# Kernel tuning notes

Measured on AMD Instinct MI355X. Metric: run time of the kernel, lower is better.

## Reference

```python
import jax, jax.numpy as jnp
import numpy as np

N = 50000      # nodes
E = 800000     # edges (before self-loops)
IN = 256       # in_dim
HID = 64       # hidden_dim per head
HEADS = 4
OUT = 256      # out_dim
NEG_SLOPE = 0.2


def setup_inputs() -> dict:
    key = jax.random.key(0)
    ks = jax.random.split(key, 12)
    s = 0.1
    return {
        "x": jax.random.normal(ks[0], (N, IN), jnp.float32),
        "edge_index": jax.random.randint(ks[1], (2, E), 0, N, dtype=jnp.int32),
        # layer 1: GATConv(IN, HID, heads=HEADS, concat=True)
        "W1": jax.random.normal(ks[2], (IN, HEADS * HID), jnp.float32) * s,
        "att_src1": jax.random.normal(ks[3], (HEADS, HID), jnp.float32) * s,
        "att_dst1": jax.random.normal(ks[4], (HEADS, HID), jnp.float32) * s,
        "b1": jnp.zeros((HEADS * HID,), jnp.float32),
        # layer 2: GATConv(HEADS*HID, OUT, heads=1, concat=False)
        "W2": jax.random.normal(ks[5], (HEADS * HID, OUT), jnp.float32) * s,
        "att_src2": jax.random.normal(ks[6], (1, OUT), jnp.float32) * s,
        "att_dst2": jax.random.normal(ks[7], (1, OUT), jnp.float32) * s,
        "b2": jnp.zeros((OUT,), jnp.float32),
    }


def _gat_layer(x, src, dst, W, a_src, a_dst, b, heads, concat):
    n = x.shape[0]
    h = (x @ W).reshape(n, heads, -1)                     # [N,H,F]
    al_s = jnp.einsum('nhf,hf->nh', h, a_src)             # [N,H]
    al_d = jnp.einsum('nhf,hf->nh', h, a_dst)
    e = jax.nn.leaky_relu(al_s[src] + al_d[dst], NEG_SLOPE)  # [E,H]
    # segment softmax over incoming edges of each dst node
    m = jax.lax.stop_gradient(jax.ops.segment_max(e, dst, num_segments=n))
    ex = jnp.exp(e - m[dst])
    denom = jax.ops.segment_sum(ex, dst, num_segments=n)
    alpha = ex / (denom[dst] + 1e-16)                     # [E,H]
    out = jax.ops.segment_sum(h[src] * alpha[:, :, None], dst, num_segments=n)  # [N,H,F]
    out = out.reshape(n, -1) if concat else out.mean(axis=1)
    return out + b


def reference(x, edge_index, W1, att_src1, att_dst1, b1, W2, att_src2, att_dst2, b2):
    n = x.shape[0]
    loop = jnp.arange(n, dtype=edge_index.dtype)
    ei = jnp.concatenate([edge_index, jnp.stack([loop, loop])], axis=1)  # add self loops
    src, dst = ei[0], ei[1]
    h = _gat_layer(x, src, dst, W1, att_src1, att_dst1, b1, HEADS, True)
    h = jax.nn.elu(h)
    out = _gat_layer(h, src, dst, W2, att_src2, att_dst2, b2, 1, False)
    return out
```

## Files before the change

kernel.cpp:

```cpp
#include <hip/hip_runtime.h>
#include <math.h>

#define IN_DIM 256
#define FDIM 256
#define HEADS 4
#define NEG 0.2f
#define MAXD 96

typedef __attribute__((ext_vector_type(8))) short bf16x8;
typedef __attribute__((ext_vector_type(8))) unsigned short u16x8;
typedef __attribute__((ext_vector_type(4))) float f32x4;

__device__ __forceinline__ float leaky(float x){ return x > 0.f ? x : NEG * x; }

__device__ __forceinline__ unsigned short f2bf(float f){
  unsigned int u = __float_as_uint(f);
  unsigned int r = u + 0x7fffu + ((u >> 16) & 1u);
  return (unsigned short)(r >> 16);
}
__device__ __forceinline__ float bf2f(unsigned short s){
  return __uint_as_float(((unsigned int)s) << 16);
}

__device__ __forceinline__ float4 bcast4(float4 v){
  return make_float4(__shfl(v.x,0,64), __shfl(v.y,0,64), __shfl(v.z,0,64), __shfl(v.w,0,64));
}
__device__ __forceinline__ float comp4(float4 v, int h){
  return h==0 ? v.x : h==1 ? v.y : h==2 ? v.z : v.w;
}

__device__ __forceinline__ void gld_lds16(const void* g, void* l){
  __builtin_amdgcn_global_load_lds((const __attribute__((address_space(1))) unsigned int*)g,
                                   (__attribute__((address_space(3))) unsigned int*)l, 16, 0, 0);
}

__global__ void k_wthist(const float* __restrict__ W1, unsigned short* __restrict__ W1t,
                         const float* __restrict__ W2, unsigned short* __restrict__ W2t,
                         const int* __restrict__ dst, int* __restrict__ deg, int E){
  int b = blockIdx.x;
  if (b < 32){
    __shared__ float tile[64][65];
    const float* W = (b < 16) ? W1 : W2;
    unsigned short* Wt = (b < 16) ? W1t : W2t;
    int bb = b & 15;
    int tk = (bb >> 2) * 64, tn = (bb & 3) * 64;
    int t = threadIdx.x;
    int cr = t >> 6, cc = t & 63;
    #pragma unroll
    for (int r = 0; r < 16; ++r){
      int k = r * 4 + cr;
      tile[k][cc] = W[(size_t)(tk + k) * 256 + tn + cc];
    }
    __syncthreads();
    #pragma unroll
    for (int r = 0; r < 16; ++r){
      int nn = r * 4 + cr;
      Wt[(size_t)(tn + nn) * 256 + tk + cc] = f2bf(tile[cc][nn]);
    }
  } else {
    int e = (b - 32) * 256 + threadIdx.x;
    if (e < E) atomicAdd(&deg[dst[e]], 1);
  }
}

__global__ void k_scanA(const int* __restrict__ deg, int* tmp, int* partials, int n){
  __shared__ int sm[256];
  int i = blockIdx.x * 256 + threadIdx.x;
  int v = (i < n) ? deg[i] + 1 : 0;
  sm[threadIdx.x] = v; __syncthreads();
  for (int off = 1; off < 256; off <<= 1){
    int x = (threadIdx.x >= off) ? sm[threadIdx.x - off] : 0;
    __syncthreads();
    sm[threadIdx.x] += x;
    __syncthreads();
  }
  if (i < n) tmp[i] = sm[threadIdx.x];
  if (threadIdx.x == 255) partials[blockIdx.x] = sm[255];
}

__global__ void k_scanC(const int* __restrict__ tmp, const int* __restrict__ deg,
                        const int* __restrict__ partials, int* rowptr, int n, int nb){
  __shared__ int ws[4];
  int bid = blockIdx.x, t = threadIdx.x;
  int lane = t & 63, w = t >> 6;
  int v = (t < bid && t < nb) ? partials[t] : 0;
  #pragma unroll
  for (int off = 32; off >= 1; off >>= 1) v += __shfl_down(v, off, 64);
  if (lane == 0) ws[w] = v;
  __syncthreads();
  int prefix = ws[0] + ws[1] + ws[2] + ws[3];
  int i = bid * 256 + t;
  if (i < n){
    int incl = tmp[i] + prefix;
    rowptr[i] = incl - (deg[i] + 1);
    if (i == n - 1) rowptr[n] = incl;
  }
}

__global__ void k_fill(const int* __restrict__ src, const int* __restrict__ dst,
                       const int* __restrict__ rowptr, int* fill, int* col, int E, int n){
  int e = blockIdx.x * blockDim.x + threadIdx.x;
  if (e < E + n){
    int s, d;
    if (e < E){ s = src[e]; d = dst[e]; } else { s = d = e - E; }
    int pos = atomicAdd(&fill[d], 1);
    col[rowptr[d] + pos] = s;
  }
}

__global__ __launch_bounds__(256) void k_gemm1(const float* __restrict__ X,
                                               const unsigned short* __restrict__ Bt,
                                               unsigned short* __restrict__ C, int n){
  __shared__ __align__(16) unsigned short sh[8192];
  unsigned short* As = sh;
  unsigned short* Bs = sh + 4096;
  int tid = threadIdx.x;
  int lane = tid & 63, wave = tid >> 6;
  int rowBase = blockIdx.x * 128, colBase = blockIdx.y * 128;
  int wr = (wave & 1) * 64, wc = (wave >> 1) * 64;

  f32x4 acc[4][4] = {};
  int c0 = tid, c1 = tid + 256;
  int r0 = c0 >> 2, kc0 = (c0 & 3) * 8;
  int r1 = c1 >> 2, kc1 = (c1 & 3) * 8;
  int m0 = lane & 15, kq = (lane >> 4) * 8;
  int ra = rowBase + r0; if (ra >= n) ra = n - 1;
  int rb = rowBase + r1; if (rb >= n) rb = n - 1;

  for (int k0 = 0; k0 < 256; k0 += 32){
    float4 va0 = *(const float4*)(X + (size_t)ra * 256 + k0 + kc0);
    float4 va1 = *(const float4*)(X + (size_t)ra * 256 + k0 + kc0 + 4);
    float4 vb0 = *(const float4*)(X + (size_t)rb * 256 + k0 + kc1);
    float4 vb1 = *(const float4*)(X + (size_t)rb * 256 + k0 + kc1 + 4);
    u16x8 sa, sb;
    sa[0]=f2bf(va0.x); sa[1]=f2bf(va0.y); sa[2]=f2bf(va0.z); sa[3]=f2bf(va0.w);
    sa[4]=f2bf(va1.x); sa[5]=f2bf(va1.y); sa[6]=f2bf(va1.z); sa[7]=f2bf(va1.w);
    sb[0]=f2bf(vb0.x); sb[1]=f2bf(vb0.y); sb[2]=f2bf(vb0.z); sb[3]=f2bf(vb0.w);
    sb[4]=f2bf(vb1.x); sb[5]=f2bf(vb1.y); sb[6]=f2bf(vb1.z); sb[7]=f2bf(vb1.w);
    *(u16x8*)(As + c0 * 8) = sa;
    *(u16x8*)(As + c1 * 8) = sb;
    gld_lds16(Bt + (size_t)(colBase + r0) * 256 + k0 + kc0, (char*)Bs + c0 * 16);
    gld_lds16(Bt + (size_t)(colBase + r1) * 256 + k0 + kc1, (char*)Bs + c1 * 16);
    __syncthreads();
    bf16x8 af[4], bfr[4];
    #pragma unroll
    for (int it = 0; it < 4; ++it)
      af[it] = *(const bf16x8*)(As + (wr + it * 16 + m0) * 32 + kq);
    #pragma unroll
    for (int jt = 0; jt < 4; ++jt)
      bfr[jt] = *(const bf16x8*)(Bs + (wc + jt * 16 + m0) * 32 + kq);
    #pragma unroll
    for (int it = 0; it < 4; ++it)
      #pragma unroll
      for (int jt = 0; jt < 4; ++jt)
        acc[it][jt] = __builtin_amdgcn_mfma_f32_16x16x32_bf16(af[it], bfr[jt], acc[it][jt], 0, 0, 0);
    __syncthreads();
  }
  int cq = lane >> 4, cm = lane & 15;
  #pragma unroll
  for (int p = 0; p < 2; ++p){
    if ((wave >> 1) == p){
      #pragma unroll
      for (int it = 0; it < 4; ++it)
        #pragma unroll
        for (int jt = 0; jt < 4; ++jt)
          #pragma unroll
          for (int r = 0; r < 4; ++r)
            sh[(wr + it * 16 + cq * 4 + r) * 64 + jt * 16 + cm] = f2bf(acc[it][jt][r]);
    }
    __syncthreads();
    #pragma unroll
    for (int q = 0; q < 4; ++q){
      int id = tid + q * 256;
      int r = id >> 3, sg = id & 7;
      u16x8 v = *(const u16x8*)(sh + r * 64 + sg * 8);
      *(u16x8*)(C + (size_t)(rowBase + r) * 256 + colBase + p * 64 + sg * 8) = v;
    }
    __syncthreads();
  }
}

__global__ __launch_bounds__(256) void k_gemm(const unsigned short* __restrict__ A,
                                              const unsigned short* __restrict__ Bt,
                                              unsigned short* __restrict__ C){
  __shared__ __align__(16) unsigned short sh[8192];
  unsigned short* As = sh;
  unsigned short* Bs = sh + 4096;
  int tid = threadIdx.x;
  int lane = tid & 63, wave = tid >> 6;
  int rowBase = blockIdx.x * 128, colBase = blockIdx.y * 128;
  int wr = (wave & 1) * 64, wc = (wave >> 1) * 64;

  f32x4 acc[4][4] = {};
  int c0 = tid, c1 = tid + 256;
  int r0 = c0 >> 2, kc0 = (c0 & 3) * 8;
  int r1 = c1 >> 2, kc1 = (c1 & 3) * 8;
  int m0 = lane & 15, kq = (lane >> 4) * 8;

  for (int k0 = 0; k0 < 256; k0 += 32){
    gld_lds16(A  + (size_t)(rowBase + r0) * 256 + k0 + kc0, (char*)As + c0 * 16);
    gld_lds16(A  + (size_t)(rowBase + r1) * 256 + k0 + kc1, (char*)As + c1 * 16);
    gld_lds16(Bt + (size_t)(colBase + r0) * 256 + k0 + kc0, (char*)Bs + c0 * 16);
    gld_lds16(Bt + (size_t)(colBase + r1) * 256 + k0 + kc1, (char*)Bs + c1 * 16);
    __syncthreads();
    bf16x8 af[4], bfr[4];
    #pragma unroll
    for (int it = 0; it < 4; ++it)
      af[it] = *(const bf16x8*)(As + (wr + it * 16 + m0) * 32 + kq);
    #pragma unroll
    for (int jt = 0; jt < 4; ++jt)
      bfr[jt] = *(const bf16x8*)(Bs + (wc + jt * 16 + m0) * 32 + kq);
    #pragma unroll
    for (int it = 0; it < 4; ++it)
      #pragma unroll
      for (int jt = 0; jt < 4; ++jt)
        acc[it][jt] = __builtin_amdgcn_mfma_f32_16x16x32_bf16(af[it], bfr[jt], acc[it][jt], 0, 0, 0);
    __syncthreads();
  }
  int cq = lane >> 4, cm = lane & 15;
  #pragma unroll
  for (int p = 0; p < 2; ++p){
    if ((wave >> 1) == p){
      #pragma unroll
      for (int it = 0; it < 4; ++it)
        #pragma unroll
        for (int jt = 0; jt < 4; ++jt)
          #pragma unroll
          for (int r = 0; r < 4; ++r)
            sh[(wr + it * 16 + cq * 4 + r) * 64 + jt * 16 + cm] = f2bf(acc[it][jt][r]);
    }
    __syncthreads();
    #pragma unroll
    for (int q = 0; q < 4; ++q){
      int id = tid + q * 256;
      int r = id >> 3, sg = id & 7;
      u16x8 v = *(const u16x8*)(sh + r * 64 + sg * 8);
      *(u16x8*)(C + (size_t)(rowBase + r) * 256 + colBase + p * 64 + sg * 8) = v;
    }
    __syncthreads();
  }
}

__global__ __launch_bounds__(256) void k_al4(const unsigned short* __restrict__ Hb,
                      const float* __restrict__ as_, const float* __restrict__ ad_,
                      float* als, float* ald, int n){
  int wave = threadIdx.x >> 6, lane = threadIdx.x & 63;
  int i = blockIdx.x * 4 + wave; if (i >= n) i = n - 1;
  int f = lane * 4;
  ushort4 hv = *(const ushort4*)(Hb + (size_t)i * FDIM + f);
  float4 av = *(const float4*)(as_ + f);
  float4 dv = *(const float4*)(ad_ + f);
  float h0 = bf2f(hv.x), h1 = bf2f(hv.y), h2 = bf2f(hv.z), h3 = bf2f(hv.w);
  float ps = h0*av.x + h1*av.y + h2*av.z + h3*av.w;
  float pd = h0*dv.x + h1*dv.y + h2*dv.z + h3*dv.w;
  #pragma unroll
  for (int off = 8; off >= 1; off >>= 1){
    ps += __shfl_down(ps, off, 16);
    pd += __shfl_down(pd, off, 16);
  }
  if ((lane & 15) == 0){
    int h = lane >> 4;
    als[i * HEADS + h] = ps; ald[i * HEADS + h] = pd;
  }
}

__global__ __launch_bounds__(256) void k_al1(const unsigned short* __restrict__ Hb,
                      const float* __restrict__ as_, const float* __restrict__ ad_,
                      float* als, float* ald, int n){
  int wave = threadIdx.x >> 6, lane = threadIdx.x & 63;
  int i = blockIdx.x * 4 + wave; if (i >= n) i = n - 1;
  int f = lane * 4;
  ushort4 hv = *(const ushort4*)(Hb + (size_t)i * FDIM + f);
  float4 av = *(const float4*)(as_ + f);
  float4 dv = *(const float4*)(ad_ + f);
  float h0 = bf2f(hv.x), h1 = bf2f(hv.y), h2 = bf2f(hv.z), h3 = bf2f(hv.w);
  float ps = h0*av.x + h1*av.y + h2*av.z + h3*av.w;
  float pd = h0*dv.x + h1*dv.y + h2*dv.z + h3*dv.w;
  #pragma unroll
  for (int off = 32; off >= 1; off >>= 1){
    ps += __shfl_down(ps, off, 64);
    pd += __shfl_down(pd, off, 64);
  }
  if (lane == 0){ als[i] = ps; ald[i] = pd; }
}

__global__ __launch_bounds__(256) void k_agg1(const unsigned short* __restrict__ Hb,
    const float* __restrict__ als, const float* __restrict__ ald,
    const int* __restrict__ rowptr, const int* __restrict__ col,
    const float* __restrict__ b, unsigned short* __restrict__ outb, int i0, int nEnd){
  __shared__ __align__(16) int   colS[4][MAXD];
  __shared__ __align__(16) float wS[4][MAXD][4];
  int wave = threadIdx.x >> 6, t = threadIdx.x & 63;
  int i = i0 + blockIdx.x * 4 + wave; if (i >= nEnd) i = nEnd - 1;
  int start = rowptr[i];
  int deg = rowptr[i + 1] - start;
  float4 adv = *(const float4*)(ald + (size_t)i * 4);
  bool staged = (deg <= MAXD);

  float4 ls = make_float4(0.f, 0.f, 0.f, 0.f);
  if (staged){
    for (int j = t; j < deg; j += 64){
      int s = col[start + j];
      colS[wave][j] = s;
      float4 a = *(const float4*)(als + (size_t)s * 4);
      float4 w = make_float4(__expf(leaky(a.x + adv.x)), __expf(leaky(a.y + adv.y)),
                             __expf(leaky(a.z + adv.z)), __expf(leaky(a.w + adv.w)));
      *(float4*)(&wS[wave][j][0]) = w;
      ls.x += w.x; ls.y += w.y; ls.z += w.z; ls.w += w.w;
    }
  } else {
    for (int j = t; j < deg; j += 64){
      int s = col[start + j];
      float4 a = *(const float4*)(als + (size_t)s * 4);
      ls.x += __expf(leaky(a.x + adv.x)); ls.y += __expf(leaky(a.y + adv.y));
      ls.z += __expf(leaky(a.z + adv.z)); ls.w += __expf(leaky(a.w + adv.w));
    }
  }
  #pragma unroll
  for (int off = 32; off >= 1; off >>= 1) ls = make_float4(
      ls.x + __shfl_down(ls.x, off, 64), ls.y + __shfl_down(ls.y, off, 64),
      ls.z + __shfl_down(ls.z, off, 64), ls.w + __shfl_down(ls.w, off, 64));
  float4 d4 = bcast4(ls);
  __syncthreads();

  int e2 = t >> 5, l32 = t & 31;
  int h = l32 >> 3, f = l32 * 8;
  float inv = 1.f / (comp4(d4, h) + 1e-16f);
  const unsigned short* Hrow = Hb + f;
  float a0[8] = {0,0,0,0,0,0,0,0}, a1[8] = {0,0,0,0,0,0,0,0};
  if (staged){
    int j = 0;
    for (; j + 3 < deg; j += 4){
      int j0 = j + e2, j1 = j + 2 + e2;
      int s0 = colS[wave][j0], s1 = colS[wave][j1];
      float w0 = wS[wave][j0][h], w1 = wS[wave][j1][h];
      u16x8 h0 = *(const u16x8*)(Hrow + (size_t)s0 * FDIM);
      u16x8 h1 = *(const u16x8*)(Hrow + (size_t)s1 * FDIM);
      #pragma unroll
      for (int k = 0; k < 8; ++k){ a0[k] += bf2f(h0[k]) * w0; a1[k] += bf2f(h1[k]) * w1; }
    }
    for (; j < deg; j += 2){
      int jj = j + e2;
      if (jj < deg){
        int s = colS[wave][jj]; float w = wS[wave][jj][h];
        u16x8 hh = *(const u16x8*)(Hrow + (size_t)s * FDIM);
        #pragma unroll
        for (int k = 0; k < 8; ++k) a0[k] += bf2f(hh[k]) * w;
      }
    }
  } else {
    float adh = comp4(adv, h);
    for (int j = e2; j < deg; j += 2){
      int s = col[start + j];
      float w = __expf(leaky(als[(size_t)s * 4 + h] + adh));
      u16x8 hh = *(const u16x8*)(Hrow + (size_t)s * FDIM);
      #pragma unroll
      for (int k = 0; k < 8; ++k) a0[k] += bf2f(hh[k]) * w;
    }
  }
  float r[8];
  #pragma unroll
  for (int k = 0; k < 8; ++k){
    r[k] = a0[k] + a1[k];
    r[k] += __shfl_down(r[k], 32, 64);
  }
  if (t < 32){
    float4 bA = *(const float4*)(b + f);
    float4 bB = *(const float4*)(b + f + 4);
    float bb[8] = {bA.x, bA.y, bA.z, bA.w, bB.x, bB.y, bB.z, bB.w};
    u16x8 o;
    #pragma unroll
    for (int k = 0; k < 8; ++k){
      float v = r[k] * inv + bb[k];
      v = (v > 0.f) ? v : (__expf(v) - 1.f);
      o[k] = f2bf(v);
    }
    *(u16x8*)(outb + (size_t)i * FDIM + f) = o;
  }
}

__global__ __launch_bounds__(256) void k_agg2(const unsigned short* __restrict__ Hb,
    const float* __restrict__ als, const float* __restrict__ ald,
    const int* __restrict__ rowptr, const int* __restrict__ col,
    const float* __restrict__ b, float* __restrict__ out, int i0, int nEnd){
  __shared__ __align__(16) int   colS[4][MAXD];
  __shared__ __align__(16) float wS[4][MAXD];
  int wave = threadIdx.x >> 6, t = threadIdx.x & 63;
  int i = i0 + blockIdx.x * 4 + wave; if (i >= nEnd) i = nEnd - 1;
  int start = rowptr[i];
  int deg = rowptr[i + 1] - start;
  float adv = ald[i];
  bool staged = (deg <= MAXD);

  float ls = 0.f;
  if (staged){
    for (int j = t; j < deg; j += 64){
      int s = col[start + j];
      colS[wave][j] = s;
      float w = __expf(leaky(als[s] + adv));
      wS[wave][j] = w;
      ls += w;
    }
  } else {
    for (int j = t; j < deg; j += 64) ls += __expf(leaky(als[col[start + j]] + adv));
  }
  #pragma unroll
  for (int off = 32; off >= 1; off >>= 1) ls += __shfl_down(ls, off, 64);
  float inv = 1.f / (__shfl(ls, 0, 64) + 1e-16f);
  __syncthreads();

  int e2 = t >> 5, l32 = t & 31;
  int f = l32 * 8;
  const unsigned short* Hrow = Hb + f;
  float a0[8] = {0,0,0,0,0,0,0,0}, a1[8] = {0,0,0,0,0,0,0,0};
  if (staged){
    int j = 0;
    for (; j + 3 < deg; j += 4){
      int j0 = j + e2, j1 = j + 2 + e2;
      int s0 = colS[wave][j0], s1 = colS[wave][j1];
      float w0 = wS[wave][j0], w1 = wS[wave][j1];
      u16x8 h0 = *(const u16x8*)(Hrow + (size_t)s0 * FDIM);
      u16x8 h1 = *(const u16x8*)(Hrow + (size_t)s1 * FDIM);
      #pragma unroll
      for (int k = 0; k < 8; ++k){ a0[k] += bf2f(h0[k]) * w0; a1[k] += bf2f(h1[k]) * w1; }
    }
    for (; j < deg; j += 2){
      int jj = j + e2;
      if (jj < deg){
        int s = colS[wave][jj]; float w = wS[wave][jj];
        u16x8 hh = *(const u16x8*)(Hrow + (size_t)s * FDIM);
        #pragma unroll
        for (int k = 0; k < 8; ++k) a0[k] += bf2f(hh[k]) * w;
      }
    }
  } else {
    for (int j = e2; j < deg; j += 2){
      int s = col[start + j];
      float w = __expf(leaky(als[s] + adv));
      u16x8 hh = *(const u16x8*)(Hrow + (size_t)s * FDIM);
      #pragma unroll
      for (int k = 0; k < 8; ++k) a0[k] += bf2f(hh[k]) * w;
    }
  }
  float r[8];
  #pragma unroll
  for (int k = 0; k < 8; ++k){
    r[k] = a0[k] + a1[k];
    r[k] += __shfl_down(r[k], 32, 64);
  }
  if (t < 32){
    float4 bA = *(const float4*)(b + f);
    float4 bB = *(const float4*)(b + f + 4);
    float4 oA = make_float4(r[0]*inv + bA.x, r[1]*inv + bA.y, r[2]*inv + bA.z, r[3]*inv + bA.w);
    float4 oB = make_float4(r[4]*inv + bB.x, r[5]*inv + bB.y, r[6]*inv + bB.z, r[7]*inv + bB.w);
    *(float4*)(out + (size_t)i * FDIM + f) = oA;
    *(float4*)(out + (size_t)i * FDIM + f + 4) = oB;
  }
}

extern "C" void kernel_launch(void* const* d_in, const int* in_sizes, int n_in,
                              void* d_out, int out_size, void* d_ws, size_t ws_size,
                              hipStream_t stream){
  const float* x   = (const float*)d_in[0];
  const int*   ei  = (const int*)d_in[1];
  const float* W1  = (const float*)d_in[2];
  const float* as1 = (const float*)d_in[3];
  const float* ad1 = (const float*)d_in[4];
  const float* b1  = (const float*)d_in[5];
  const float* W2  = (const float*)d_in[6];
  const float* as2 = (const float*)d_in[7];
  const float* ad2 = (const float*)d_in[8];
  const float* b2  = (const float*)d_in[9];
  float* out = (float*)d_out;

  int n = in_sizes[0] / IN_DIM;
  int E = in_sizes[1] / 2;
  int Mpad = (n + 127) & ~127;
  const int* srcIdx = ei;
  const int* dstIdx = ei + E;

  char* ws = (char*)d_ws;
  size_t off = 0;
  auto alloc = [&](size_t bytes) -> void* {
    void* p = ws + off; off += (bytes + 255) & ~(size_t)255; return p;
  };
  unsigned short* bufA = (unsigned short*)alloc((size_t)Mpad * FDIM * 2);
  unsigned short* bufB = (unsigned short*)alloc((size_t)Mpad * FDIM * 2);
  unsigned short* W1t  = (unsigned short*)alloc(256 * 256 * 2);
  unsigned short* W2t  = (unsigned short*)alloc(256 * 256 * 2);
  int*   zeros    = (int*)alloc((size_t)n * 2 * 4);
  int*   deg      = zeros;
  int*   fill     = zeros + n;
  int*   tmp      = (int*)alloc((size_t)n * 4);
  int*   rowptr   = (int*)alloc((size_t)(n + 1) * 4);
  int*   partials = (int*)alloc(1024 * 4);
  int*   col      = (int*)alloc((size_t)(E + n) * 4);
  float* als1     = (float*)alloc((size_t)n * HEADS * 4);
  float* ald1     = (float*)alloc((size_t)n * HEADS * 4);
  float* als2     = (float*)alloc((size_t)n * 4);
  float* ald2     = (float*)alloc((size_t)n * 4);
  (void)ws_size;

  int nb = (n + 255) / 256;
  hipMemsetAsync(zeros, 0, (size_t)n * 2 * 4, stream);

  int histBlocks = (E + 255) / 256;
  k_wthist<<<32 + histBlocks, 256, 0, stream>>>(W1, W1t, W2, W2t, dstIdx, deg, E);

  k_scanA<<<nb, 256, 0, stream>>>(deg, tmp, partials, n);
  k_scanC<<<nb, 256, 0, stream>>>(tmp, deg, partials, rowptr, n, nb);
  k_fill<<<(E + n + 255) / 256, 256, 0, stream>>>(srcIdx, dstIdx, rowptr, fill, col, E, n);

  dim3 gg(Mpad / 128, FDIM / 128);
  int ga = (n + 3) / 4;
  int nA = 25000;
  int gaA = nA / 4, gaB = (n - nA + 3) / 4;
  k_gemm1<<<gg, 256, 0, stream>>>(x, W1t, bufB, n);
  k_al4<<<ga, 256, 0, stream>>>(bufB, as1, ad1, als1, ald1, n);
  k_agg1<<<gaA, 256, 0, stream>>>(bufB, als1, ald1, rowptr, col, b1, bufA, 0, nA);
  k_agg1<<<gaB, 256, 0, stream>>>(bufB, als1, ald1, rowptr, col, b1, bufA, nA, n);
  k_gemm<<<gg, 256, 0, stream>>>(bufA, W2t, bufB);
  k_al1<<<ga, 256, 0, stream>>>(bufB, as2, ad2, als2, ald2, n);
  k_agg2<<<gaA, 256, 0, stream>>>(bufB, als2, ald2, rowptr, col, b2, out, 0, nA);
  k_agg2<<<gaB, 256, 0, stream>>>(bufB, als2, ald2, rowptr, col, b2, out, nA, n);
}
```

Before: 400.5 us.

## Fuse GEMM1 with degree histogram and CSR fill with attention logits

Splits weight transposition into its own kernel, then merges the first GEMM with the degree-histogram atomics in one grid, and merges the CSR fill with the layer-1 attention-logit computation. The fill is restructured so each block scans a chunk of edges eight times, once per destination-range team, which localizes atomics and column writes to a node range. The intent is to cut launch count and overlap independent work, at the cost of each edge being read eight times and atomics contending with the GEMM.

```diff
diff --git a/kernel.cpp b/kernel.cpp
--- a/kernel.cpp
+++ b/kernel.cpp
@@ -6,6 +6,7 @@
 #define HEADS 4
 #define NEG 0.2f
 #define MAXD 96
+#define CPB 2048
 
 typedef __attribute__((ext_vector_type(8))) short bf16x8;
 typedef __attribute__((ext_vector_type(8))) unsigned short u16x8;
@@ -34,89 +35,46 @@
                                    (__attribute__((address_space(3))) unsigned int*)l, 16, 0, 0);
 }
 
-__global__ void k_wthist(const float* __restrict__ W1, unsigned short* __restrict__ W1t,
-                         const float* __restrict__ W2, unsigned short* __restrict__ W2t,
-                         const int* __restrict__ dst, int* __restrict__ deg, int E){
+__global__ void k_wt(const float* __restrict__ W1, unsigned short* __restrict__ W1t,
+                     const float* __restrict__ W2, unsigned short* __restrict__ W2t){
+  __shared__ float tile[64][65];
   int b = blockIdx.x;
-  if (b < 32){
-    __shared__ float tile[64][65];
-    const float* W = (b < 16) ? W1 : W2;
-    unsigned short* Wt = (b < 16) ? W1t : W2t;
-    int bb = b & 15;
-    int tk = (bb >> 2) * 64, tn = (bb & 3) * 64;
-    int t = threadIdx.x;
-    int cr = t >> 6, cc = t & 63;
-    #pragma unroll
-    for (int r = 0; r < 16; ++r){
-      int k = r * 4 + cr;
-      tile[k][cc] = W[(size_t)(tk + k) * 256 + tn + cc];
-    }
-    __syncthreads();
-    #pragma unroll
-    for (int r = 0; r < 16; ++r){
-      int nn = r * 4 + cr;
-      Wt[(size_t)(tn + nn) * 256 + tk + cc] = f2bf(tile[cc][nn]);
-    }
-  } else {
-    int e = (b - 32) * 256 + threadIdx.x;
+  const float* W = (b < 16) ? W1 : W2;
+  unsigned short* Wt = (b < 16) ? W1t : W2t;
+  int bb = b & 15;
+  int tk = (bb >> 2) * 64, tn = (bb & 3) * 64;
+  int t = threadIdx.x;
+  int cr = t >> 6, cc = t & 63;
+  #pragma unroll
+  for (int r = 0; r < 16; ++r){
+    int k = r * 4 + cr;
+    tile[k][cc] = W[(size_t)(tk + k) * 256 + tn + cc];
+  }
+  __syncthreads();
+  #pragma unroll
+  for (int r = 0; r < 16; ++r){
+    int nn = r * 4 + cr;
+    Wt[(size_t)(tn + nn) * 256 + tk + cc] = f2bf(tile[cc][nn]);
+  }
+}
+
+__global__ __launch_bounds__(256) void k_g1h(const float* __restrict__ X,
+                                             const unsigned short* __restrict__ Bt,
+                                             unsigned short* __restrict__ C, int n, int nbx,
+                                             const int* __restrict__ dst, int* __restrict__ deg, int E){
+  int b = blockIdx.x;
+  int gemmB = 2 * nbx;
+  if (b >= gemmB){
+    int e = (b - gemmB) * 256 + threadIdx.x;
     if (e < E) atomicAdd(&deg[dst[e]], 1);
-  }
-}
-
-__global__ void k_scanA(const int* __restrict__ deg, int* tmp, int* partials, int n){
-  __shared__ int sm[256];
-  int i = blockIdx.x * 256 + threadIdx.x;
-  int v = (i < n) ? deg[i] + 1 : 0;
-  sm[threadIdx.x] = v; __syncthreads();
-  for (int off = 1; off < 256; off <<= 1){
-    int x = (threadIdx.x >= off) ? sm[threadIdx.x - off] : 0;
-    __syncthreads();
-    sm[threadIdx.x] += x;
-    __syncthreads();
-  }
-  if (i < n) tmp[i] = sm[threadIdx.x];
-  if (threadIdx.x == 255) partials[blockIdx.x] = sm[255];
-}
-
-__global__ void k_scanC(const int* __restrict__ tmp, const int* __restrict__ deg,
-                        const int* __restrict__ partials, int* rowptr, int n, int nb){
-  __shared__ int ws[4];
-  int bid = blockIdx.x, t = threadIdx.x;
-  int lane = t & 63, w = t >> 6;
-  int v = (t < bid && t < nb) ? partials[t] : 0;
-  #pragma unroll
-  for (int off = 32; off >= 1; off >>= 1) v += __shfl_down(v, off, 64);
-  if (lane == 0) ws[w] = v;
-  __syncthreads();
-  int prefix = ws[0] + ws[1] + ws[2] + ws[3];
-  int i = bid * 256 + t;
-  if (i < n){
-    int incl = tmp[i] + prefix;
-    rowptr[i] = incl - (deg[i] + 1);
-    if (i == n - 1) rowptr[n] = incl;
-  }
-}
-
-__global__ void k_fill(const int* __restrict__ src, const int* __restrict__ dst,
-                       const int* __restrict__ rowptr, int* fill, int* col, int E, int n){
-  int e = blockIdx.x * blockDim.x + threadIdx.x;
-  if (e < E + n){
-    int s, d;
-    if (e < E){ s = src[e]; d = dst[e]; } else { s = d = e - E; }
-    int pos = atomicAdd(&fill[d], 1);
-    col[rowptr[d] + pos] = s;
-  }
-}
-
-__global__ __launch_bounds__(256) void k_gemm1(const float* __restrict__ X,
-                                               const unsigned short* __restrict__ Bt,
-                                               unsigned short* __restrict__ C, int n){
+    return;
+  }
   __shared__ __align__(16) unsigned short sh[8192];
   unsigned short* As = sh;
   unsigned short* Bs = sh + 4096;
   int tid = threadIdx.x;
   int lane = tid & 63, wave = tid >> 6;
-  int rowBase = blockIdx.x * 128, colBase = blockIdx.y * 128;
+  int rowBase = (b % nbx) * 128, colBase = (b / nbx) * 128;
   int wr = (wave & 1) * 64, wc = (wave >> 1) * 64;
 
   f32x4 acc[4][4] = {};
@@ -180,6 +138,84 @@
   }
 }
 
+__global__ void k_scanA(const int* __restrict__ deg, int* tmp, int* partials, int n){
+  __shared__ int sm[256];
+  int i = blockIdx.x * 256 + threadIdx.x;
+  int v = (i < n) ? deg[i] + 1 : 0;
+  sm[threadIdx.x] = v; __syncthreads();
+  for (int off = 1; off < 256; off <<= 1){
+    int x = (threadIdx.x >= off) ? sm[threadIdx.x - off] : 0;
+    __syncthreads();
+    sm[threadIdx.x] += x;
+    __syncthreads();
+  }
+  if (i < n) tmp[i] = sm[threadIdx.x];
+  if (threadIdx.x == 255) partials[blockIdx.x] = sm[255];
+}
+
+__global__ void k_scanC(const int* __restrict__ tmp, const int* __restrict__ deg,
+                        const int* __restrict__ partials, int* rowptr, int n, int nb){
+  __shared__ int ws[4];
+  int bid = blockIdx.x, t = threadIdx.x;
+  int lane = t & 63, w = t >> 6;
+  int v = (t < bid && t < nb) ? partials[t] : 0;
+  #pragma unroll
+  for (int off = 32; off >= 1; off >>= 1) v += __shfl_down(v, off, 64);
+  if (lane == 0) ws[w] = v;
+  __syncthreads();
+  int prefix = ws[0] + ws[1] + ws[2] + ws[3];
+  int i = bid * 256 + t;
+  if (i < n){
+    int incl = tmp[i] + prefix;
+    rowptr[i] = incl - (deg[i] + 1);
+    if (i == n - 1) rowptr[n] = incl;
+  }
+}
+
+__global__ __launch_bounds__(256) void k_fillal4(const int* __restrict__ src, const int* __restrict__ dst,
+    const int* __restrict__ rowptr, int* fill, int* col, int E, int n, int fillB,
+    const unsigned short* __restrict__ Hb, const float* __restrict__ as_, const float* __restrict__ ad_,
+    float* als, float* ald){
+  int b = blockIdx.x;
+  if (b < fillB){
+    int team = b & 7, chunk = b >> 3;
+    int span = (n + 7) >> 3;
+    int lo = team * span, hi = lo + span; if (hi > n) hi = n;
+    int base = chunk * CPB + threadIdx.x;
+    #pragma unroll
+    for (int it = 0; it < CPB / 256; ++it){
+      int e = base + it * 256;
+      if (e < E + n){
+        int d = (e < E) ? dst[e] : e - E;
+        if (d >= lo && d < hi){
+          int s = (e < E) ? src[e] : d;
+          int pos = atomicAdd(&fill[d], 1);
+          col[rowptr[d] + pos] = s;
+        }
+      }
+    }
+    return;
+  }
+  int wave = threadIdx.x >> 6, lane = threadIdx.x & 63;
+  int i = (b - fillB) * 4 + wave; if (i >= n) i = n - 1;
+  int f = lane * 4;
+  ushort4 hv = *(const ushort4*)(Hb + (size_t)i * FDIM + f);
+  float4 av = *(const float4*)(as_ + f);
+  float4 dv = *(const float4*)(ad_ + f);
+  float h0 = bf2f(hv.x), h1 = bf2f(hv.y), h2 = bf2f(hv.z), h3 = bf2f(hv.w);
+  float ps = h0*av.x + h1*av.y + h2*av.z + h3*av.w;
+  float pd = h0*dv.x + h1*dv.y + h2*dv.z + h3*dv.w;
+  #pragma unroll
+  for (int off = 8; off >= 1; off >>= 1){
+    ps += __shfl_down(ps, off, 16);
+    pd += __shfl_down(pd, off, 16);
+  }
+  if ((lane & 15) == 0){
+    int h = lane >> 4;
+    als[i * HEADS + h] = ps; ald[i * HEADS + h] = pd;
+  }
+}
+
 __global__ __launch_bounds__(256) void k_gemm(const unsigned short* __restrict__ A,
                                               const unsigned short* __restrict__ Bt,
                                               unsigned short* __restrict__ C){
@@ -238,29 +274,6 @@
       *(u16x8*)(C + (size_t)(rowBase + r) * 256 + colBase + p * 64 + sg * 8) = v;
     }
     __syncthreads();
-  }
-}
-
-__global__ __launch_bounds__(256) void k_al4(const unsigned short* __restrict__ Hb,
-                      const float* __restrict__ as_, const float* __restrict__ ad_,
-                      float* als, float* ald, int n){
-  int wave = threadIdx.x >> 6, lane = threadIdx.x & 63;
-  int i = blockIdx.x * 4 + wave; if (i >= n) i = n - 1;
-  int f = lane * 4;
-  ushort4 hv = *(const ushort4*)(Hb + (size_t)i * FDIM + f);
-  float4 av = *(const float4*)(as_ + f);
-  float4 dv = *(const float4*)(ad_ + f);
-  float h0 = bf2f(hv.x), h1 = bf2f(hv.y), h2 = bf2f(hv.z), h3 = bf2f(hv.w);
-  float ps = h0*av.x + h1*av.y + h2*av.z + h3*av.w;
-  float pd = h0*dv.x + h1*dv.y + h2*dv.z + h3*dv.w;
-  #pragma unroll
-  for (int off = 8; off >= 1; off >>= 1){
-    ps += __shfl_down(ps, off, 16);
-    pd += __shfl_down(pd, off, 16);
-  }
-  if ((lane & 15) == 0){
-    int h = lane >> 4;
-    als[i * HEADS + h] = ps; ald[i * HEADS + h] = pd;
   }
 }
 
@@ -502,23 +515,28 @@
   (void)ws_size;
 
   int nb = (n + 255) / 256;
+  int nbx = Mpad / 128;
   hipMemsetAsync(zeros, 0, (size_t)n * 2 * 4, stream);
 
+  k_wt<<<32, 256, 0, stream>>>(W1, W1t, W2, W2t);
+
   int histBlocks = (E + 255) / 256;
-  k_wthist<<<32 + histBlocks, 256, 0, stream>>>(W1, W1t, W2, W2t, dstIdx, deg, E);
+  k_g1h<<<2 * nbx + histBlocks, 256, 0, stream>>>(x, W1t, bufB, n, nbx, dstIdx, deg, E);
 
   k_scanA<<<nb, 256, 0, stream>>>(deg, tmp, partials, n);
   k_scanC<<<nb, 256, 0, stream>>>(tmp, deg, partials, rowptr, n, nb);
-  k_fill<<<(E + n + 255) / 256, 256, 0, stream>>>(srcIdx, dstIdx, rowptr, fill, col, E, n);
-
-  dim3 gg(Mpad / 128, FDIM / 128);
+
   int ga = (n + 3) / 4;
+  int fillChunks = (E + n + CPB - 1) / CPB;
+  int fillB = fillChunks * 8;
+  k_fillal4<<<fillB + ga, 256, 0, stream>>>(srcIdx, dstIdx, rowptr, fill, col, E, n, fillB,
+                                            bufB, as1, ad1, als1, ald1);
+
   int nA = 25000;
   int gaA = nA / 4, gaB = (n - nA + 3) / 4;
-  k_gemm1<<<gg, 256, 0, stream>>>(x, W1t, bufB, n);
-  k_al4<<<ga, 256, 0, stream>>>(bufB, as1, ad1, als1, ald1, n);
   k_agg1<<<gaA, 256, 0, stream>>>(bufB, als1, ald1, rowptr, col, b1, bufA, 0, nA);
   k_agg1<<<gaB, 256, 0, stream>>>(bufB, als1, ald1, rowptr, col, b1, bufA, nA, n);
+  dim3 gg(nbx, 2);
   k_gemm<<<gg, 256, 0, stream>>>(bufA, W2t, bufB);
   k_al1<<<ga, 256, 0, stream>>>(bufB, as2, ad2, als2, ald2, n);
   k_agg2<<<gaA, 256, 0, stream>>>(bufB, als2, ald2, rowptr, col, b2, out, 0, nA);
```

Result: faster. 376.6 us (-6.0%).
